# Performance work log

Measured on AMD Instinct MI355X. Metric: run time of the kernel, lower is better.

The kernel has to match this reference:

```python
import jax, jax.numpy as jnp
import numpy as np

DN = ('NCHW', 'OIHW', 'NCHW')

def conv2d(x, w, pad):
    return jax.lax.conv_general_dilated(x, w, (1, 1), [(pad, pad), (pad, pad)], dimension_numbers=DN)

def conv_module(x, w, g, b):
    # Conv2d -> BN (inference-mode per-channel affine) -> ReLU
    pad = (w.shape[-1] - 1) // 2
    y = conv2d(x, w, pad)
    return jax.nn.relu(y * g[None, :, None, None] + b[None, :, None, None])

def seq_conv_module(x, w, g, b):
    # x: (T, B, C, H, W) -> apply ConvModule per frame by folding T into batch
    T, B, C, H, W = x.shape
    y = conv_module(x.reshape(T * B, C, H, W), w, g, b)
    return y.reshape(T, B, -1, H, W)

def setup_inputs() -> dict:
    key = jax.random.key(0)
    ks = jax.random.split(key, 32)
    Cin, Ck, Cv, Cout = 1024, 256, 512, 512
    T, B, H, W = 4, 1, 64, 64
    s = 0.02
    d = {}
    d['x'] = jax.random.normal(ks[0], (B, Cin, H, W), jnp.float32)
    d['seq'] = jax.random.normal(ks[1], (T, B, Cin, H, W), jnp.float32)
    def mk_cm(i, cin, cout, k):
        return (jax.random.normal(ks[i], (cout, cin, k, k), jnp.float32) * s,
                jnp.ones((cout,), jnp.float32),
                jnp.zeros((cout,), jnp.float32))
    d['wk1'], d['gk1'], d['bk1'] = mk_cm(2, Cin, Ck, 1)
    d['wk2'], d['gk2'], d['bk2'] = mk_cm(3, Ck, Ck, 3)
    d['wv1'], d['gv1'], d['bv1'] = mk_cm(4, Cin, Cv, 1)
    d['wv2'], d['gv2'], d['bv2'] = mk_cm(5, Cv, Cv, 3)
    d['wqk1'], d['gqk1'], d['bqk1'] = mk_cm(6, Cin, Ck, 1)
    d['wqk2'], d['gqk2'], d['bqk2'] = mk_cm(7, Ck, Ck, 3)
    d['wqv1'], d['gqv1'], d['bqv1'] = mk_cm(8, Cin, Cv, 1)
    d['wqv2'], d['gqv2'], d['bqv2'] = mk_cm(9, Cv, Cv, 3)
    d['wb'], d['gb'], d['bb'] = mk_cm(10, 2 * Cv, Cout, 3)
    return d

def reference(x, seq, wk1, gk1, bk1, wk2, gk2, bk2, wv1, gv1, bv1, wv2, gv2, bv2,
              wqk1, gqk1, bqk1, wqk2, gqk2, bqk2, wqv1, gqv1, bqv1, wqv2, gqv2, bqv2,
              wb, gb, bb):
    # memory key/value convs over the T reference frames
    mk = seq_conv_module(seq_conv_module(seq, wk1, gk1, bk1), wk2, gk2, bk2)  # (T,B,Ck,H,W)
    mv = seq_conv_module(seq_conv_module(seq, wv1, gv1, bv1), wv2, gv2, bv2)  # (T,B,Cv,H,W)
    # query key/value convs on current frame
    qk = conv_module(conv_module(x, wqk1, gqk1, bqk1), wqk2, gqk2, bqk2)      # (B,Ck,H,W)
    qv = conv_module(conv_module(x, wqv1, gqv1, bqv1), wqv2, gqv2, bqv2)      # (B,Cv,H,W)
    T, B, Ck, H, W = mk.shape
    Cv = mv.shape[2]
    mk = jnp.transpose(mk, (1, 2, 0, 3, 4)).reshape(B, Ck, T * H * W)         # (B,Ck,THW)
    mv = jnp.transpose(mv, (1, 2, 0, 3, 4)).reshape(B, Cv, T * H * W)         # (B,Cv,THW)
    qkf = qk.reshape(B, Ck, H * W)                                            # (B,Ck,HW)
    # attention: (B,HW,THW); matmul_norm=False so no 1/sqrt(Ck) scaling
    attn = jax.nn.softmax(jnp.einsum('bcq,bck->bqk', qkf, mk), axis=-1)
    mem = jnp.einsum('bqk,bck->bcq', attn, mv).reshape(B, Cv, H, W)
    out = conv_module(jnp.concatenate([qv, mem], axis=1), wb, gb, bb)
    return out
```

## Files before the change

### kernel.cpp

```cpp
#include <hip/hip_runtime.h>
#include <stdint.h>


typedef short bf16x8 __attribute__((ext_vector_type(8)));
typedef float f32x4  __attribute__((ext_vector_type(4)));
typedef unsigned short u16x4 __attribute__((ext_vector_type(4)));

__device__ __forceinline__ unsigned short f2bf(float f) {
  union { float f; unsigned u; } x; x.f = f;
  unsigned r = x.u + 0x7FFFu + ((x.u >> 16) & 1u);
  return (unsigned short)(r >> 16);
}

typedef const __attribute__((address_space(1))) char* as1cp;
typedef __attribute__((address_space(3))) char* as3p;

__device__ __forceinline__ void gl_lds16(const char* g, char* l) {
  __builtin_amdgcn_global_load_lds((as1cp)g, (as3p)l, 16, 0, 0);
}

template<bool CF, bool CONV3, bool XTILED>
__global__ __launch_bounds__(512, 2) void gemm256(
    const unsigned short* __restrict__ Wp,
    const unsigned short* __restrict__ Xp,
    int K, int Kc, int Xstride, int Xcoloff, int cin_log2,
    float* __restrict__ P, int Mtot, size_t plane,
    const char* __restrict__ zp)
{
  __shared__ short Ap[2][2][8192];
  __shared__ short Bp[2][2][8192];
  const int tid = threadIdx.x;
  const int w = tid >> 6;
  const int l = tid & 63;
  const int wm_idx = w >> 2;
  const int wn_idx = w & 3;
  const int n0 = blockIdx.x * 256;
  const int m0 = blockIdx.y * 256;
  const int wrow0 = CF ? n0 : m0;
  const int xrow0 = CF ? m0 : n0;

  const int g = (l & 7) ^ (l >> 3);
  const int grow0 = w * 32 + 2 * (l >> 3) + (g >> 2);
  const int gc = g & 3;

  auto srcW = [&](int grow, int h, int k0) -> const char* {
    return (const char*)Wp +
           (((size_t)(wrow0 + grow)) * K + (size_t)(k0 + h * 32 + gc * 8)) * 2;
  };
  auto srcX = [&](int grow, int h, int k0) -> const char* {
    if constexpr (XTILED) {
      return (const char*)Xp + (size_t)((k0 + h * 32) >> 5) * ((size_t)Xstride * 64)
             + (size_t)(xrow0 + grow) * 64 + gc * 16;
    } else if constexpr (CONV3) {
      int e = k0 >> cin_log2;
      int ci0 = k0 & ((1 << cin_log2) - 1);
      int kh = e / 3, kw = e - kh * 3;
      int dpos = (kh - 1) * 64 + (kw - 1);
      int p = xrow0 + grow;
      int hw = p & 4095;
      int h2 = (hw >> 6) + kh - 1, w2 = (hw & 63) + kw - 1;
      return ((unsigned)h2 < 64u && (unsigned)w2 < 64u)
          ? (const char*)Xp + (((size_t)(p + dpos)) * Xstride
                               + (size_t)(Xcoloff + ci0 + h * 32 + gc * 8)) * 2
          : zp + gc * 16;
    } else {
      return (const char*)Xp + (((size_t)(xrow0 + grow)) * Xstride
                                + (size_t)(Xcoloff + k0 + h * 32 + gc * 8)) * 2;
    }
  };

  auto stage_half = [&](int b, int h, int k0) {
#pragma unroll
    for (int j = 0; j < 2; j++) {
      int grow = grow0 + j * 16;
      const char* sm = CF ? srcX(grow, h, k0) : srcW(grow, h, k0);
      gl_lds16(sm, (char*)&Ap[b][h][0] + w * 2048 + j * 1024);
    }
#pragma unroll
    for (int j = 0; j < 2; j++) {
      int grow = grow0 + j * 16;
      const char* sn = CF ? srcW(grow, h, k0) : srcX(grow, h, k0);
      gl_lds16(sn, (char*)&Bp[b][h][0] + w * 2048 + j * 1024);
    }
  };

  auto rd = [&](const short* base, int row, int ks) -> bf16x8 {
    int R = row >> 1;
    int sp = (((row & 1) << 2) | ks) ^ (R & 7);
    return *(const bf16x8*)(base + R * 64 + sp * 8);
  };

  f32x4 acc[8][4] = {};

  const int kb = blockIdx.z * Kc;
  const int NT = Kc >> 6;

  stage_half(0, 0, kb);
  stage_half(0, 1, kb);
  asm volatile("s_waitcnt vmcnt(4)" ::: "memory");
  __builtin_amdgcn_s_barrier();

  int buf = 0;
  for (int t = 0; t < NT; ++t) {
    int k0n = kb + (t + 1) * 64;
    bool pre = (t + 1 < NT);
#pragma unroll
    for (int h = 0; h < 2; ++h) {
      const short* Am = &Ap[buf][h][0];
      const short* Bm = &Bp[buf][h][0];
      bf16x8 af[8], bfv[4];
#pragma unroll
      for (int i = 0; i < 8; i++)
        af[i] = rd(Am, wm_idx * 128 + i * 16 + (l & 15), l >> 4);
#pragma unroll
      for (int j = 0; j < 4; j++)
        bfv[j] = rd(Bm, wn_idx * 64 + j * 16 + (l & 15), l >> 4);
      if (pre) stage_half(buf ^ 1, h, k0n);
      __builtin_amdgcn_s_setprio(1);
#pragma unroll
      for (int i = 0; i < 8; i++)
#pragma unroll
        for (int j = 0; j < 4; j++)
          acc[i][j] = __builtin_amdgcn_mfma_f32_16x16x32_bf16(af[i], bfv[j], acc[i][j], 0, 0, 0);
      __builtin_amdgcn_s_setprio(0);
      if (pre) asm volatile("s_waitcnt vmcnt(4)" ::: "memory");
      else     asm volatile("s_waitcnt vmcnt(0)" ::: "memory");
      __builtin_amdgcn_s_barrier();
    }
    buf ^= 1;
  }

  float* Pz = P + (size_t)blockIdx.z * plane;
  const int col = l & 15;
  const int rb2 = (l >> 4) << 2;
#pragma unroll
  for (int j = 0; j < 4; j++) {
    int gn = n0 + wn_idx * 64 + j * 16 + col;
#pragma unroll
    for (int i = 0; i < 8; i++) {
      int gm = m0 + wm_idx * 128 + i * 16 + rb2;
      *(f32x4*)(Pz + (size_t)gn * Mtot + gm) = acc[i][j];
    }
  }
}

enum { EP_CL_BNR = 0, EP_CF_BNR_BF16 = 1, EP_CF_BNR_F32 = 2, EP_EXPSUM = 3,
       EP_PVDIV = 4, EP_PART = 5 };

template<int EP, bool CF, bool CONV3, bool XTILED>
__global__ __launch_bounds__(256) void gemm_k(
    const unsigned short* __restrict__ Wp,
    const unsigned short* __restrict__ Xp,
    int K, int Kc, int Xstride, int Xcoloff, int cin_log2,
    void* __restrict__ Op, int Ostride, int Ocoloff, size_t plane,
    const float* __restrict__ g1, const float* __restrict__ b1,
    const float* __restrict__ g2, const float* __restrict__ b2, int gsplit,
    float* __restrict__ rowsum, const char* __restrict__ zp)
{
  __shared__ short Wt[2][128 * 32];
  __shared__ short Xt[2][128 * 32];
  const int tid = threadIdx.x;
  const int w = tid >> 6;
  const int l = tid & 63;
  const int m0 = blockIdx.y * 128;
  const int n0 = blockIdx.x * 128;
  const int wrow0 = CF ? n0 : m0;
  const int xrow0 = CF ? m0 : n0;

  const int ch0 = w, ch1 = w + 4;
  const int sr0 = ch0 * 16 + (l >> 2);
  const int sr1 = ch1 * 16 + (l >> 2);
  const int kbp = (l & 3) << 4;
  const int kbl0 = kbp ^ ((sr0 & 3) << 4);
  const int kbl1 = kbp ^ ((sr1 & 3) << 4);

  const size_t wrb = (size_t)K * 2;
  const size_t xrb = (size_t)Xstride * 2;

  const int wm = (w >> 1) * 64;
  const int wn = (w & 1) * 64;

  const int k_begin = blockIdx.z * Kc;
  const int k_end = (k_begin + Kc < K) ? (k_begin + Kc) : K;

  auto stage = [&](int b, int k0) {
    int ci0 = k0, kh = 1, kw = 1, dpos = 0;
    if (CONV3) {
      int e = k0 >> cin_log2;
      ci0 = k0 & ((1 << cin_log2) - 1);
      kh = e / 3; kw = e - kh * 3;
      dpos = (kh - 1) * 64 + (kw - 1);
    }
    char* Wl = (char*)&Wt[b][0];
    char* Xl = (char*)&Xt[b][0];
    gl_lds16((const char*)Wp + (size_t)(wrow0 + sr0) * wrb + (size_t)k0 * 2 + kbl0,
             Wl + ch0 * 1024);
    gl_lds16((const char*)Wp + (size_t)(wrow0 + sr1) * wrb + (size_t)k0 * 2 + kbl1,
             Wl + ch1 * 1024);
    const char* xs0;
    const char* xs1;
    if constexpr (XTILED) {
      size_t kslab = (size_t)(k0 >> 5) * ((size_t)Xstride * 64);
      xs0 = (const char*)Xp + kslab + (size_t)(xrow0 + sr0) * 64 + kbl0;
      xs1 = (const char*)Xp + kslab + (size_t)(xrow0 + sr1) * 64 + kbl1;
    } else if constexpr (CONV3) {
      int p = xrow0 + sr0;
      int hw = p & 4095;
      int h2 = (hw >> 6) + kh - 1, w2 = (hw & 63) + kw - 1;
      xs0 = ((unsigned)h2 < 64u && (unsigned)w2 < 64u)
          ? (const char*)Xp + (size_t)(p + dpos) * xrb + (size_t)(Xcoloff + ci0) * 2 + kbl0
          : zp + kbl0;
      p = xrow0 + sr1;
      hw = p & 4095;
      h2 = (hw >> 6) + kh - 1; w2 = (hw & 63) + kw - 1;
      xs1 = ((unsigned)h2 < 64u && (unsigned)w2 < 64u)
          ? (const char*)Xp + (size_t)(p + dpos) * xrb + (size_t)(Xcoloff + ci0) * 2 + kbl1
          : zp + kbl1;
    } else {
      xs0 = (const char*)Xp + (size_t)(xrow0 + sr0) * xrb + (size_t)(Xcoloff + k0) * 2 + kbl0;
      xs1 = (const char*)Xp + (size_t)(xrow0 + sr1) * xrb + (size_t)(Xcoloff + k0) * 2 + kbl1;
    }
    gl_lds16(xs0, Xl + ch0 * 1024);
    gl_lds16(xs1, Xl + ch1 * 1024);
  };

  f32x4 acc[4][4] = {};

  int cur = 0;
  stage(0, k_begin);
  for (int k0 = k_begin; k0 < k_end; k0 += 32) {
    if (k0 + 32 < k_end) {
      stage(cur ^ 1, k0 + 32);
      asm volatile("s_waitcnt vmcnt(4)" ::: "memory");
    } else {
      asm volatile("s_waitcnt vmcnt(0)" ::: "memory");
    }
    __builtin_amdgcn_s_barrier();

    const short* Wb = &Wt[cur][0];
    const short* Xb = &Xt[cur][0];
    const short* At = CF ? Xb : Wb;
    const short* Bt = CF ? Wb : Xb;

    bf16x8 af[4], bfv[4];
#pragma unroll
    for (int i = 0; i < 4; i++) {
      int row = wm + i * 16 + (l & 15);
      int kb = ((l >> 4) << 4) ^ ((row & 3) << 4);
      af[i] = *(const bf16x8*)(At + row * 32 + (kb >> 1));
    }
#pragma unroll
    for (int j = 0; j < 4; j++) {
      int row = wn + j * 16 + (l & 15);
      int kb = ((l >> 4) << 4) ^ ((row & 3) << 4);
      bfv[j] = *(const bf16x8*)(Bt + row * 32 + (kb >> 1));
    }
#pragma unroll
    for (int i = 0; i < 4; i++)
#pragma unroll
      for (int j = 0; j < 4; j++)
        acc[i][j] = __builtin_amdgcn_mfma_f32_16x16x32_bf16(af[i], bfv[j], acc[i][j], 0, 0, 0);

    __builtin_amdgcn_s_barrier();
    cur ^= 1;
  }

  const int col = l & 15;
  const int rb = (l >> 4) << 2;

  if constexpr (EP == EP_PART) {
    float* P = (float*)Op + (size_t)blockIdx.z * plane;
#pragma unroll
    for (int j = 0; j < 4; j++) {
      int gn = n0 + wn + j * 16 + col;
#pragma unroll
      for (int i = 0; i < 4; i++) {
        int gm = m0 + wm + i * 16 + rb;
        *(f32x4*)(P + (size_t)gn * Ostride + gm) = acc[i][j];
      }
    }
  }
  if constexpr (EP == EP_CL_BNR) {
#pragma unroll
    for (int i = 0; i < 4; i++) {
      int gm = m0 + wm + i * 16 + rb;
      const float* gp; const float* bp;
      if (gm < gsplit) { gp = g1 + gm; bp = b1 + gm; }
      else             { gp = g2 + (gm - gsplit); bp = b2 + (gm - gsplit); }
      float G[4], B[4];
#pragma unroll
      for (int r = 0; r < 4; r++) { G[r] = gp[r]; B[r] = bp[r]; }
#pragma unroll
      for (int j = 0; j < 4; j++) {
        int gn = n0 + wn + j * 16 + col;
        f32x4 v = acc[i][j];
        u16x4 o;
#pragma unroll
        for (int r = 0; r < 4; r++) o[r] = f2bf(fmaxf(v[r] * G[r] + B[r], 0.f));
        *(u16x4*)((unsigned short*)Op + (size_t)gn * Ostride + Ocoloff + gm) = o;
      }
    }
  }
  if constexpr (EP == EP_CF_BNR_BF16 || EP == EP_CF_BNR_F32) {
#pragma unroll
    for (int j = 0; j < 4; j++) {
      int gn = n0 + wn + j * 16 + col;
      float G = (gn < gsplit) ? g1[gn] : g2[gn - gsplit];
      float Bv = (gn < gsplit) ? b1[gn] : b2[gn - gsplit];
#pragma unroll
      for (int i = 0; i < 4; i++) {
        int gm = m0 + wm + i * 16 + rb;
        f32x4 v = acc[i][j];
        if constexpr (EP == EP_CF_BNR_F32) {
          f32x4 o;
#pragma unroll
          for (int r = 0; r < 4; r++) o[r] = fmaxf(v[r] * G + Bv, 0.f);
          *(f32x4*)((float*)Op + (size_t)gn * Ostride + Ocoloff + gm) = o;
        } else {
          u16x4 o;
#pragma unroll
          for (int r = 0; r < 4; r++) o[r] = f2bf(fmaxf(v[r] * G + Bv, 0.f));
          *(u16x4*)((unsigned short*)Op + (size_t)gn * Ostride + Ocoloff + gm) = o;
        }
      }
    }
  }
  if constexpr (EP == EP_EXPSUM) {
#pragma unroll
    for (int j = 0; j < 4; j++) {
      int gn = n0 + wn + j * 16 + col;
      float s = 0.f;
#pragma unroll
      for (int i = 0; i < 4; i++) {
        int gm = m0 + wm + i * 16 + rb;
        f32x4 v = acc[i][j];
        u16x4 o;
#pragma unroll
        for (int r = 0; r < 4; r++) { float e = __expf(v[r]); s += e; o[r] = f2bf(e); }
        if (gsplit)
          *(u16x4*)((unsigned short*)Op + (size_t)(gm >> 5) * ((size_t)Ostride * 32)
                    + (size_t)gn * 32 + (gm & 31)) = o;
        else
          *(u16x4*)((unsigned short*)Op + (size_t)gn * Ostride + gm) = o;
      }
      s += __shfl_xor(s, 16);
      s += __shfl_xor(s, 32);
      if (l < 16) atomicAdd(rowsum + gn, s);
    }
  }
  if constexpr (EP == EP_PVDIV) {
#pragma unroll
    for (int j = 0; j < 4; j++) {
      int gn = n0 + wn + j * 16 + col;
      float inv = 1.0f / rowsum[gn];
#pragma unroll
      for (int i = 0; i < 4; i++) {
        int gm = m0 + wm + i * 16 + rb;
        f32x4 v = acc[i][j];
        u16x4 o;
#pragma unroll
        for (int r = 0; r < 4; r++) o[r] = f2bf(v[r] * inv);
        *(u16x4*)((unsigned short*)Op + (size_t)gn * Ostride + Ocoloff + gm) = o;
      }
    }
  }
}

enum { RED_BNR_BF16 = 0, RED_PVDIV = 1, RED_BNR_F32 = 2, RED_BNR_BF16_N = 3 };

template<int MODE>
__global__ __launch_bounds__(256) void reduce_k(
    const float* __restrict__ P, int Z, size_t plane, int Cdim,
    void* __restrict__ out, int Ostride, int Ocoloff,
    const float* __restrict__ g1, const float* __restrict__ b1,
    const float* __restrict__ g2, const float* __restrict__ b2, int gsplit,
    const float* __restrict__ rowsum, int total4)
{
  int t = blockIdx.x * 256 + threadIdx.x;
  if (t >= total4) return;
  size_t base = (size_t)t * 4;
  int n = (int)(base / (size_t)Cdim);
  int c = (int)(base % (size_t)Cdim);
  f32x4 s = *(const f32x4*)(P + base);
  for (int z = 1; z < Z; z++) {
    f32x4 v = *(const f32x4*)(P + (size_t)z * plane + base);
    s += v;
  }
  if constexpr (MODE == RED_BNR_BF16) {
    u16x4 o;
#pragma unroll
    for (int r = 0; r < 4; r++) {
      int ch = c + r;
      float G = (ch < gsplit) ? g1[ch] : g2[ch - gsplit];
      float B = (ch < gsplit) ? b1[ch] : b2[ch - gsplit];
      o[r] = f2bf(fmaxf(s[r] * G + B, 0.f));
    }
    *(u16x4*)((unsigned short*)out + (size_t)n * Ostride + Ocoloff + c) = o;
  }
  if constexpr (MODE == RED_BNR_BF16_N) {
    float G = g1[n], B = b1[n];
    u16x4 o;
#pragma unroll
    for (int r = 0; r < 4; r++) o[r] = f2bf(fmaxf(s[r] * G + B, 0.f));
    *(u16x4*)((unsigned short*)out + (size_t)n * Ostride + Ocoloff + c) = o;
  }
  if constexpr (MODE == RED_PVDIV) {
    float inv = 1.0f / rowsum[n];
    u16x4 o;
#pragma unroll
    for (int r = 0; r < 4; r++) o[r] = f2bf(s[r] * inv);
    *(u16x4*)((unsigned short*)out + (size_t)n * Ostride + Ocoloff + c) = o;
  }
  if constexpr (MODE == RED_BNR_F32) {
    float G = g1[n], B = b1[n];
    f32x4 o;
#pragma unroll
    for (int r = 0; r < 4; r++) o[r] = fmaxf(s[r] * G + B, 0.f);
    *(f32x4*)((float*)out + (size_t)n * Ostride + c) = o;
  }
}

__global__ __launch_bounds__(256) void nchw_to_cl(const float* __restrict__ src,
                                                  unsigned short* __restrict__ dst,
                                                  int C, int P) {
  __shared__ float t[32][33];
  int f = blockIdx.z;
  src += (size_t)f * C * P;
  dst += (size_t)f * C * P;
  int p0 = blockIdx.x * 32, c0 = blockIdx.y * 32;
  int a = threadIdx.x & 31, b = threadIdx.x >> 5;
#pragma unroll
  for (int k = 0; k < 4; k++)
    t[b + 8 * k][a] = src[(size_t)(c0 + b + 8 * k) * P + p0 + a];
  __syncthreads();
#pragma unroll
  for (int k = 0; k < 4; k++)
    dst[(size_t)(p0 + b + 8 * k) * C + c0 + a] = f2bf(t[a][b + 8 * k]);
}

__global__ __launch_bounds__(256) void cvt_bf16(const float* __restrict__ s,
                                                unsigned short* __restrict__ d, int n) {
  int i = blockIdx.x * 256 + threadIdx.x;
  if (i < n) d[i] = f2bf(s[i]);
}

__global__ __launch_bounds__(256) void repack3(const float* __restrict__ s,
                                               unsigned short* __restrict__ d,
                                               int ci_log2, int n) {
  int i = blockIdx.x * 256 + threadIdx.x;
  if (i >= n) return;
  int Ci = 1 << ci_log2;
  int ci = i & (Ci - 1);
  int t = i >> ci_log2;
  int e = t % 9;
  int co = t / 9;
  d[i] = f2bf(s[((size_t)co * Ci + ci) * 9 + e]);
}

__global__ __launch_bounds__(256) void fillf(float* p, float v, int n) {
  int i = blockIdx.x * 256 + threadIdx.x;
  if (i < n) p[i] = v;
}

extern "C" void kernel_launch(void* const* d_in, const int* in_sizes, int n_in,
                              void* d_out, int out_size, void* d_ws, size_t ws_size,
                              hipStream_t stream) {
  (void)in_sizes; (void)n_in;
  const float* x    = (const float*)d_in[0];
  const float* seq  = (const float*)d_in[1];
  const float* wk1  = (const float*)d_in[2];
  const float* gk1  = (const float*)d_in[3];
  const float* bk1  = (const float*)d_in[4];
  const float* wk2  = (const float*)d_in[5];
  const float* gk2  = (const float*)d_in[6];
  const float* bk2  = (const float*)d_in[7];
  const float* wv1  = (const float*)d_in[8];
  const float* gv1  = (const float*)d_in[9];
  const float* bv1  = (const float*)d_in[10];
  const float* wv2  = (const float*)d_in[11];
  const float* gv2  = (const float*)d_in[12];
  const float* bv2  = (const float*)d_in[13];
  const float* wqk1 = (const float*)d_in[14];
  const float* gqk1 = (const float*)d_in[15];
  const float* bqk1 = (const float*)d_in[16];
  const float* wqk2 = (const float*)d_in[17];
  const float* gqk2 = (const float*)d_in[18];
  const float* bqk2 = (const float*)d_in[19];
  const float* wqv1 = (const float*)d_in[20];
  const float* gqv1 = (const float*)d_in[21];
  const float* bqv1 = (const float*)d_in[22];
  const float* wqv2 = (const float*)d_in[23];
  const float* gqv2 = (const float*)d_in[24];
  const float* bqv2 = (const float*)d_in[25];
  const float* wb   = (const float*)d_in[26];
  const float* gb   = (const float*)d_in[27];
  const float* bb   = (const float*)d_in[28];

  char* ws = (char*)d_ws;
  size_t off = 0;
  auto alloc = [&](size_t bytes) { size_t o = off; off += (bytes + 255) & ~(size_t)255; return o; };
  size_t o_zp    = alloc(4096);
  size_t o_rs    = alloc(4096 * 4);
  size_t o_wKV1  = alloc((size_t)768 * 1024 * 2);
  size_t o_wQKV1 = alloc((size_t)768 * 1024 * 2);
  size_t o_wK2   = alloc((size_t)256 * 2304 * 2);
  size_t o_wQK2  = alloc((size_t)256 * 2304 * 2);
  size_t o_wV2   = alloc((size_t)512 * 4608 * 2);
  size_t o_wQV2  = alloc((size_t)512 * 4608 * 2);
  size_t o_wB    = alloc((size_t)512 * 9216 * 2);
  size_t o_mk    = alloc((size_t)16384 * 256 * 2);
  size_t o_mv    = alloc((size_t)512 * 16384 * 2);
  size_t o_qk    = alloc((size_t)4096 * 256 * 2);
  size_t o_qvm   = alloc((size_t)4096 * 1024 * 2);
  size_t o_part  = alloc((size_t)8 * 4096 * 512 * 4);
  size_t o_vol   = off;
  size_t o_xT    = o_vol;
  size_t o_seqT  = o_xT + (size_t)4096 * 1024 * 2;
  size_t o_kv1   = o_seqT + (size_t)4 * 4096 * 1024 * 2;
  size_t o_qkv1  = o_kv1 + (size_t)16384 * 768 * 2;
  size_t end1    = o_qkv1 + (size_t)4096 * 768 * 2;
  size_t o_expS  = o_vol;
  size_t end2    = o_expS + (size_t)4096 * 16384 * 2;
  size_t need    = end1 > end2 ? end1 : end2;

  bool SPLIT = ws_size >= need;
  if (!SPLIT) {
    size_t save = o_part;
    o_vol  = save;
    o_xT   = o_vol;
    o_seqT = o_xT + (size_t)4096 * 1024 * 2;
    o_kv1  = o_seqT + (size_t)4 * 4096 * 1024 * 2;
    o_qkv1 = o_kv1 + (size_t)16384 * 768 * 2;
    end1   = o_qkv1 + (size_t)4096 * 768 * 2;
    o_expS = o_vol;
    end2   = o_expS + (size_t)4096 * 16384 * 2;
    need   = end1 > end2 ? end1 : end2;
    if (ws_size < need) {
      fillf<<<(out_size + 255) / 256, 256, 0, stream>>>((float*)d_out, 12345.0f, out_size);
      return;
    }
  }

  const char* zp = ws + o_zp;
  float* rs = (float*)(ws + o_rs);
  unsigned short* wKV1p  = (unsigned short*)(ws + o_wKV1);
  unsigned short* wQKV1p = (unsigned short*)(ws + o_wQKV1);
  unsigned short* wK2p   = (unsigned short*)(ws + o_wK2);
  unsigned short* wQK2p  = (unsigned short*)(ws + o_wQK2);
  unsigned short* wV2p   = (unsigned short*)(ws + o_wV2);
  unsigned short* wQV2p  = (unsigned short*)(ws + o_wQV2);
  unsigned short* wBp    = (unsigned short*)(ws + o_wB);
  unsigned short* mkp    = (unsigned short*)(ws + o_mk);
  unsigned short* mvp    = (unsigned short*)(ws + o_mv);
  unsigned short* qkp    = (unsigned short*)(ws + o_qk);
  unsigned short* qvmp   = (unsigned short*)(ws + o_qvm);
  float* partp           = (float*)(ws + o_part);
  unsigned short* xTp    = (unsigned short*)(ws + o_xT);
  unsigned short* seqTp  = (unsigned short*)(ws + o_seqT);
  unsigned short* kv1p   = (unsigned short*)(ws + o_kv1);
  unsigned short* qkv1p  = (unsigned short*)(ws + o_qkv1);
  unsigned short* expSp  = (unsigned short*)(ws + o_expS);

  hipMemsetAsync(ws + o_zp, 0, 4096, stream);
  hipMemsetAsync(ws + o_rs, 0, 4096 * 4, stream);

  cvt_bf16<<<(256 * 1024 + 255) / 256, 256, 0, stream>>>(wk1, wKV1p, 256 * 1024);
  cvt_bf16<<<(512 * 1024 + 255) / 256, 256, 0, stream>>>(wv1, wKV1p + 256 * 1024, 512 * 1024);
  cvt_bf16<<<(256 * 1024 + 255) / 256, 256, 0, stream>>>(wqk1, wQKV1p, 256 * 1024);
  cvt_bf16<<<(512 * 1024 + 255) / 256, 256, 0, stream>>>(wqv1, wQKV1p + 256 * 1024, 512 * 1024);
  repack3<<<(256 * 2304 + 255) / 256, 256, 0, stream>>>(wk2, wK2p, 8, 256 * 2304);
  repack3<<<(256 * 2304 + 255) / 256, 256, 0, stream>>>(wqk2, wQK2p, 8, 256 * 2304);
  repack3<<<(512 * 4608 + 255) / 256, 256, 0, stream>>>(wv2, wV2p, 9, 512 * 4608);
  repack3<<<(512 * 4608 + 255) / 256, 256, 0, stream>>>(wqv2, wQV2p, 9, 512 * 4608);
  repack3<<<(512 * 9216 + 255) / 256, 256, 0, stream>>>(wb, wBp, 10, 512 * 9216);

  nchw_to_cl<<<dim3(128, 32, 1), 256, 0, stream>>>(x, xTp, 1024, 4096);
  nchw_to_cl<<<dim3(128, 32, 4), 256, 0, stream>>>(seq, seqTp, 1024, 4096);

  gemm_k<EP_CL_BNR, false, false, false><<<dim3(128, 6), 256, 0, stream>>>(
      wKV1p, seqTp, 1024, 1024, 1024, 0, 0, kv1p, 768, 0, 0,
      gk1, bk1, gv1, bv1, 256, rs, zp);

  if (SPLIT) {
    {
      size_t plane = (size_t)4096 * 768;
      gemm_k<EP_PART, false, false, false><<<dim3(32, 6, 4), 256, 0, stream>>>(
          wQKV1p, xTp, 1024, 256, 1024, 0, 0, partp, 768, 0, plane,
          nullptr, nullptr, nullptr, nullptr, 0, rs, zp);
      int t4 = (int)(plane / 4);
      reduce_k<RED_BNR_BF16><<<(t4 + 255) / 256, 256, 0, stream>>>(
          partp, 4, plane, 768, qkv1p, 768, 0, gqk1, bqk1, gqv1, bqv1, 256, rs, t4);
    }
    {
      size_t plane = (size_t)16384 * 256;
      gemm256<false, true, false><<<dim3(64, 1, 4), 512, 0, stream>>>(
          wK2p, kv1p, 2304, 576, 768, 0, 8, partp, 256, plane, zp);
      int t4 = (int)(plane / 4);
      reduce_k<RED_BNR_BF16><<<(t4 + 255) / 256, 256, 0, stream>>>(
          partp, 4, plane, 256, mkp, 256, 0, gk2, bk2, gk2, bk2, 256, rs, t4);
    }
    {
      size_t plane = (size_t)4096 * 256;
      gemm_k<EP_PART, false, true, false><<<dim3(32, 2, 8), 256, 0, stream>>>(
          wQK2p, qkv1p, 2304, 288, 768, 0, 8, partp, 256, 0, plane,
          nullptr, nullptr, nullptr, nullptr, 0, rs, zp);
      int t4 = (int)(plane / 4);
      reduce_k<RED_BNR_BF16><<<(t4 + 255) / 256, 256, 0, stream>>>(
          partp, 8, plane, 256, qkp, 256, 0, gqk2, bqk2, gqk2, bqk2, 256, rs, t4);
    }
    {
      size_t plane = (size_t)4096 * 512;
      gemm256<false, true, false><<<dim3(16, 2, 8), 512, 0, stream>>>(
          wQV2p, qkv1p, 4608, 576, 768, 256, 9, partp, 512, plane, zp);
      int t4 = (int)(plane / 4);
      reduce_k<RED_BNR_BF16><<<(t4 + 255) / 256, 256, 0, stream>>>(
          partp, 8, plane, 512, qvmp, 1024, 0, gqv2, bqv2, gqv2, bqv2, 512, rs, t4);
    }
    {
      size_t plane = (size_t)512 * 16384;
      gemm256<true, true, false><<<dim3(2, 64, 2), 512, 0, stream>>>(
          wV2p, kv1p, 4608, 2304, 768, 256, 9, partp, 16384, plane, zp);
      int t4 = (int)(plane / 4);
      reduce_k<RED_BNR_BF16_N><<<(t4 + 255) / 256, 256, 0, stream>>>(
          partp, 2, plane, 16384, mvp, 16384, 0, gv2, bv2, nullptr, nullptr, 0, rs, t4);
    }
    gemm_k<EP_EXPSUM, false, false, false><<<dim3(32, 128), 256, 0, stream>>>(
        mkp, qkp, 256, 256, 256, 0, 0, expSp, 4096, 0, 0,
        nullptr, nullptr, nullptr, nullptr, 1, rs, zp);
    {
      size_t plane = (size_t)4096 * 512;
      gemm256<false, false, true><<<dim3(16, 2, 8), 512, 0, stream>>>(
          mvp, expSp, 16384, 2048, 4096, 0, 0, partp, 512, plane, zp);
      int t4 = (int)(plane / 4);
      reduce_k<RED_PVDIV><<<(t4 + 255) / 256, 256, 0, stream>>>(
          partp, 8, plane, 512, qvmp, 1024, 512, nullptr, nullptr, nullptr, nullptr, 0, rs, t4);
    }
    {
      size_t plane = (size_t)512 * 4096;
      gemm256<true, true, false><<<dim3(2, 16, 8), 512, 0, stream>>>(
          wBp, qvmp, 9216, 1152, 1024, 0, 10, partp, 4096, plane, zp);
      int t4 = (int)(plane / 4);
      reduce_k<RED_BNR_F32><<<(t4 + 255) / 256, 256, 0, stream>>>(
          partp, 8, plane, 4096, (float*)d_out, 4096, 0, gb, bb, gb, bb, 512, rs, t4);
    }
  } else {
    gemm_k<EP_CL_BNR, false, false, false><<<dim3(32, 6), 256, 0, stream>>>(
        wQKV1p, xTp, 1024, 1024, 1024, 0, 0, qkv1p, 768, 0, 0,
        gqk1, bqk1, gqv1, bqv1, 256, rs, zp);
    gemm_k<EP_CL_BNR, false, true, false><<<dim3(128, 2), 256, 0, stream>>>(
        wK2p, kv1p, 2304, 2304, 768, 0, 8, mkp, 256, 0, 0,
        gk2, bk2, gk2, bk2, 256, rs, zp);
    gemm_k<EP_CL_BNR, false, true, false><<<dim3(32, 2), 256, 0, stream>>>(
        wQK2p, qkv1p, 2304, 2304, 768, 0, 8, qkp, 256, 0, 0,
        gqk2, bqk2, gqk2, bqk2, 256, rs, zp);
    gemm_k<EP_CL_BNR, false, true, false><<<dim3(32, 4), 256, 0, stream>>>(
        wQV2p, qkv1p, 4608, 4608, 768, 256, 9, qvmp, 1024, 0, 0,
        gqv2, bqv2, gqv2, bqv2, 512, rs, zp);
    gemm_k<EP_CF_BNR_BF16, true, true, false><<<dim3(4, 128), 256, 0, stream>>>(
        wV2p, kv1p, 4608, 4608, 768, 256, 9, mvp, 16384, 0, 0,
        gv2, bv2, gv2, bv2, 512, rs, zp);
    gemm_k<EP_EXPSUM, false, false, false><<<dim3(32, 128), 256, 0, stream>>>(
        mkp, qkp, 256, 256, 256, 0, 0, expSp, 16384, 0, 0,
        nullptr, nullptr, nullptr, nullptr, 0, rs, zp);
    gemm_k<EP_PVDIV, false, false, false><<<dim3(32, 4), 256, 0, stream>>>(
        mvp, expSp, 16384, 16384, 16384, 0, 0, qvmp, 1024, 512, 0,
        nullptr, nullptr, nullptr, nullptr, 0, rs, zp);
    gemm_k<EP_CF_BNR_F32, true, true, false><<<dim3(4, 32), 256, 0, stream>>>(
        wBp, qvmp, 9216, 9216, 1024, 0, 10, (float*)d_out, 4096, 0, 0,
        gb, bb, gb, bb, 512, rs, zp);
  }
}
```

Baseline: 564.8 us.

## Extend 256-tile GEMM with fused epilogues and XCD-aware block remap

Adds templated epilogues to the 256x256 GEMM kernel: a BN+ReLU bf16 channels-last store, and an exp/rowsum store in the tiled layout. The big KV 1x1 conv and the QK^T exp-sum GEMM now use the larger tile kernel. The QKV 1x1 conv drops its split-K partial-and-reduce pass and writes its output directly. Block IDs are remapped so consecutive tiles land on the same XCD, aiming for better L2 reuse. Risks include lower occupancy or fewer blocks for the small grids, and more atomics per row.

```diff
diff --git a/kernel.cpp b/kernel.cpp
--- a/kernel.cpp
+++ b/kernel.cpp
@@ -19,13 +19,17 @@
   __builtin_amdgcn_global_load_lds((as1cp)g, (as3p)l, 16, 0, 0);
 }
 
-template<bool CF, bool CONV3, bool XTILED>
+enum { G_PART = 0, G_CL = 1, G_EXPSUM = 2 };
+
+template<int EP, bool CF, bool CONV3, bool XTILED>
 __global__ __launch_bounds__(512, 2) void gemm256(
     const unsigned short* __restrict__ Wp,
     const unsigned short* __restrict__ Xp,
     int K, int Kc, int Xstride, int Xcoloff, int cin_log2,
-    float* __restrict__ P, int Mtot, size_t plane,
-    const char* __restrict__ zp)
+    void* __restrict__ Op, int Ostride, size_t plane,
+    const float* __restrict__ g1, const float* __restrict__ b1,
+    const float* __restrict__ g2, const float* __restrict__ b2, int gsplit,
+    float* __restrict__ rowsum, const char* __restrict__ zp)
 {
   __shared__ short Ap[2][2][8192];
   __shared__ short Bp[2][2][8192];
@@ -34,8 +38,19 @@
   const int l = tid & 63;
   const int wm_idx = w >> 2;
   const int wn_idx = w & 3;
-  const int n0 = blockIdx.x * 256;
-  const int m0 = blockIdx.y * 256;
+
+  int bx = blockIdx.x, by = blockIdx.y;
+  {
+    int nwg = gridDim.x * gridDim.y;
+    if ((nwg & 7) == 0) {
+      int id = bx + gridDim.x * by;
+      id = (id & 7) * (nwg >> 3) + (id >> 3);
+      bx = id % gridDim.x;
+      by = id / gridDim.x;
+    }
+  }
+  const int n0 = bx * 256;
+  const int m0 = by * 256;
   const int wrow0 = CF ? n0 : m0;
   const int xrow0 = CF ? m0 : n0;
 
@@ -130,16 +145,60 @@
     buf ^= 1;
   }
 
-  float* Pz = P + (size_t)blockIdx.z * plane;
   const int col = l & 15;
   const int rb2 = (l >> 4) << 2;
-#pragma unroll
-  for (int j = 0; j < 4; j++) {
-    int gn = n0 + wn_idx * 64 + j * 16 + col;
+
+  if constexpr (EP == G_PART) {
+    float* Pz = (float*)Op + (size_t)blockIdx.z * plane;
+#pragma unroll
+    for (int j = 0; j < 4; j++) {
+      int gn = n0 + wn_idx * 64 + j * 16 + col;
+#pragma unroll
+      for (int i = 0; i < 8; i++) {
+        int gm = m0 + wm_idx * 128 + i * 16 + rb2;
+        *(f32x4*)(Pz + (size_t)gn * Ostride + gm) = acc[i][j];
+      }
+    }
+  }
+  if constexpr (EP == G_CL) {
 #pragma unroll
     for (int i = 0; i < 8; i++) {
       int gm = m0 + wm_idx * 128 + i * 16 + rb2;
-      *(f32x4*)(Pz + (size_t)gn * Mtot + gm) = acc[i][j];
+      const float* gp; const float* bp;
+      if (gm < gsplit) { gp = g1 + gm; bp = b1 + gm; }
+      else             { gp = g2 + (gm - gsplit); bp = b2 + (gm - gsplit); }
+      float G[4], B[4];
+#pragma unroll
+      for (int r = 0; r < 4; r++) { G[r] = gp[r]; B[r] = bp[r]; }
+#pragma unroll
+      for (int j = 0; j < 4; j++) {
+        int gn = n0 + wn_idx * 64 + j * 16 + col;
+        f32x4 v = acc[i][j];
+        u16x4 o;
+#pragma unroll
+        for (int r = 0; r < 4; r++) o[r] = f2bf(fmaxf(v[r] * G[r] + B[r], 0.f));
+        *(u16x4*)((unsigned short*)Op + (size_t)gn * Ostride + gm) = o;
+      }
+    }
+  }
+  if constexpr (EP == G_EXPSUM) {
+#pragma unroll
+    for (int j = 0; j < 4; j++) {
+      int gn = n0 + wn_idx * 64 + j * 16 + col;
+      float s = 0.f;
+#pragma unroll
+      for (int i = 0; i < 8; i++) {
+        int gm = m0 + wm_idx * 128 + i * 16 + rb2;
+        f32x4 v = acc[i][j];
+        u16x4 o;
+#pragma unroll
+        for (int r = 0; r < 4; r++) { float e = __expf(v[r]); s += e; o[r] = f2bf(e); }
+        *(u16x4*)((unsigned short*)Op + (size_t)(gm >> 5) * ((size_t)Ostride * 32)
+                  + (size_t)gn * 32 + (gm & 31)) = o;
+      }
+      s += __shfl_xor(s, 16);
+      s += __shfl_xor(s, 32);
+      if (l < 16) atomicAdd(rowsum + gn, s);
     }
   }
 }
@@ -577,24 +636,18 @@
   nchw_to_cl<<<dim3(128, 32, 1), 256, 0, stream>>>(x, xTp, 1024, 4096);
   nchw_to_cl<<<dim3(128, 32, 4), 256, 0, stream>>>(seq, seqTp, 1024, 4096);
 
-  gemm_k<EP_CL_BNR, false, false, false><<<dim3(128, 6), 256, 0, stream>>>(
-      wKV1p, seqTp, 1024, 1024, 1024, 0, 0, kv1p, 768, 0, 0,
-      gk1, bk1, gv1, bv1, 256, rs, zp);
-
   if (SPLIT) {
-    {
-      size_t plane = (size_t)4096 * 768;
-      gemm_k<EP_PART, false, false, false><<<dim3(32, 6, 4), 256, 0, stream>>>(
-          wQKV1p, xTp, 1024, 256, 1024, 0, 0, partp, 768, 0, plane,
-          nullptr, nullptr, nullptr, nullptr, 0, rs, zp);
-      int t4 = (int)(plane / 4);
-      reduce_k<RED_BNR_BF16><<<(t4 + 255) / 256, 256, 0, stream>>>(
-          partp, 4, plane, 768, qkv1p, 768, 0, gqk1, bqk1, gqv1, bqv1, 256, rs, t4);
-    }
+    gemm256<G_CL, false, false, false><<<dim3(64, 3), 512, 0, stream>>>(
+        wKV1p, seqTp, 1024, 1024, 1024, 0, 0, kv1p, 768, 0,
+        gk1, bk1, gv1, bv1, 256, rs, zp);
+    gemm_k<EP_CL_BNR, false, false, false><<<dim3(32, 6), 256, 0, stream>>>(
+        wQKV1p, xTp, 1024, 1024, 1024, 0, 0, qkv1p, 768, 0, 0,
+        gqk1, bqk1, gqv1, bqv1, 256, rs, zp);
     {
       size_t plane = (size_t)16384 * 256;
-      gemm256<false, true, false><<<dim3(64, 1, 4), 512, 0, stream>>>(
-          wK2p, kv1p, 2304, 576, 768, 0, 8, partp, 256, plane, zp);
+      gemm256<G_PART, false, true, false><<<dim3(64, 1, 4), 512, 0, stream>>>(
+          wK2p, kv1p, 2304, 576, 768, 0, 8, partp, 256, plane,
+          nullptr, nullptr, nullptr, nullptr, 0, rs, zp);
       int t4 = (int)(plane / 4);
       reduce_k<RED_BNR_BF16><<<(t4 + 255) / 256, 256, 0, stream>>>(
           partp, 4, plane, 256, mkp, 256, 0, gk2, bk2, gk2, bk2, 256, rs, t4);
@@ -610,40 +663,47 @@
     }
     {
       size_t plane = (size_t)4096 * 512;
-      gemm256<false, true, false><<<dim3(16, 2, 8), 512, 0, stream>>>(
-          wQV2p, qkv1p, 4608, 576, 768, 256, 9, partp, 512, plane, zp);
+      gemm256<G_PART, false, true, false><<<dim3(16, 2, 8), 512, 0, stream>>>(
+          wQV2p, qkv1p, 4608, 576, 768, 256, 9, partp, 512, plane,
+          nullptr, nullptr, nullptr, nullptr, 0, rs, zp);
       int t4 = (int)(plane / 4);
       reduce_k<RED_BNR_BF16><<<(t4 + 255) / 256, 256, 0, stream>>>(
           partp, 8, plane, 512, qvmp, 1024, 0, gqv2, bqv2, gqv2, bqv2, 512, rs, t4);
     }
     {
       size_t plane = (size_t)512 * 16384;
-      gemm256<true, true, false><<<dim3(2, 64, 2), 512, 0, stream>>>(
-          wV2p, kv1p, 4608, 2304, 768, 256, 9, partp, 16384, plane, zp);
+      gemm256<G_PART, true, true, false><<<dim3(2, 64, 2), 512, 0, stream>>>(
+          wV2p, kv1p, 4608, 2304, 768, 256, 9, partp, 16384, plane,
+          nullptr, nullptr, nullptr, nullptr, 0, rs, zp);
       int t4 = (int)(plane / 4);
       reduce_k<RED_BNR_BF16_N><<<(t4 + 255) / 256, 256, 0, stream>>>(
           partp, 2, plane, 16384, mvp, 16384, 0, gv2, bv2, nullptr, nullptr, 0, rs, t4);
     }
-    gemm_k<EP_EXPSUM, false, false, false><<<dim3(32, 128), 256, 0, stream>>>(
-        mkp, qkp, 256, 256, 256, 0, 0, expSp, 4096, 0, 0,
-        nullptr, nullptr, nullptr, nullptr, 1, rs, zp);
+    gemm256<G_EXPSUM, false, false, false><<<dim3(16, 64), 512, 0, stream>>>(
+        mkp, qkp, 256, 256, 256, 0, 0, expSp, 4096, 0,
+        nullptr, nullptr, nullptr, nullptr, 0, rs, zp);
     {
       size_t plane = (size_t)4096 * 512;
-      gemm256<false, false, true><<<dim3(16, 2, 8), 512, 0, stream>>>(
-          mvp, expSp, 16384, 2048, 4096, 0, 0, partp, 512, plane, zp);
+      gemm256<G_PART, false, false, true><<<dim3(16, 2, 8), 512, 0, stream>>>(
+          mvp, expSp, 16384, 2048, 4096, 0, 0, partp, 512, plane,
+          nullptr, nullptr, nullptr, nullptr, 0, rs, zp);
       int t4 = (int)(plane / 4);
       reduce_k<RED_PVDIV><<<(t4 + 255) / 256, 256, 0, stream>>>(
           partp, 8, plane, 512, qvmp, 1024, 512, nullptr, nullptr, nullptr, nullptr, 0, rs, t4);
     }
     {
       size_t plane = (size_t)512 * 4096;
-      gemm256<true, true, false><<<dim3(2, 16, 8), 512, 0, stream>>>(
-          wBp, qvmp, 9216, 1152, 1024, 0, 10, partp, 4096, plane, zp);
+      gemm256<G_PART, true, true, false><<<dim3(2, 16, 8), 512, 0, stream>>>(
+          wBp, qvmp, 9216, 1152, 1024, 0, 10, partp, 4096, plane,
+          nullptr, nullptr, nullptr, nullptr, 0, rs, zp);
       int t4 = (int)(plane / 4);
       reduce_k<RED_BNR_F32><<<(t4 + 255) / 256, 256, 0, stream>>>(
           partp, 8, plane, 4096, (float*)d_out, 4096, 0, gb, bb, gb, bb, 512, rs, t4);
     }
   } else {
+    gemm_k<EP_CL_BNR, false, false, false><<<dim3(128, 6), 256, 0, stream>>>(
+        wKV1p, seqTp, 1024, 1024, 1024, 0, 0, kv1p, 768, 0, 0,
+        gk1, bk1, gv1, bv1, 256, rs, zp);
     gemm_k<EP_CL_BNR, false, false, false><<<dim3(32, 6), 256, 0, stream>>>(
         wQKV1p, xTp, 1024, 1024, 1024, 0, 0, qkv1p, 768, 0, 0,
         gqk1, bqk1, gqv1, bqv1, 256, rs, zp);
```

New measurement: 555.8 us (median of 2 runs). About the same (-1.6%).
